# Kernel optimization log

Hardware: AMD Instinct MI355X
Metric: run time of the kernel (lower is better)

The kernel has to match this reference:

```python
import jax, jax.numpy as jnp
import numpy as np
import math

N_BREAKPOINTS = 4
V_ORDER = 2
W_ORDER = N_BREAKPOINTS - 1
B, T, C = 32, 4096, 32


def setup_inputs() -> dict:
    key = jax.random.key(0)
    k1, k2, k3 = jax.random.split(key, 3)
    x = jax.random.normal(k1, (B, T, C), dtype=jnp.float32)
    v = jax.random.normal(k2, (C, V_ORDER, T), dtype=jnp.float32)
    w = jax.random.normal(k3, (C, W_ORDER, T), dtype=jnp.float32)
    return {"x": x, "v": v, "w": w}


def reference(x, v, w):
    # x: (B, T, C); v: (C, V_ORDER, T); w: (C, W_ORDER, T)
    Bv, Tv, Cv = x.shape
    # breakpoints = T / w_order * i, i = 0..n_breakpoints-1 (as in build())
    bp = (jnp.arange(N_BREAKPOINTS, dtype=jnp.float32) * (float(Tv) / W_ORDER))
    k_lo = bp[:-1]  # (W_ORDER,) left breakpoint k_{j-1}
    k_hi = bp[1:]   # (W_ORDER,) right breakpoint k_j

    # sigma1: sum_j v[c,j,t] * x^j / j!
    powers = jnp.stack(
        [x ** j / jnp.float32(math.factorial(j)) for j in range(V_ORDER)], axis=-1
    )  # (B, T, C, V_ORDER)
    sigma1 = jnp.einsum("btcj,cjt->btc", powers, v)

    # sigma2: piecewise quadratic basis per spline segment
    xb = x[..., None]  # (B, T, C, 1)
    f1 = 0.5 * (xb - k_lo) ** 2                               # x^2/2 - k_lo*x + k_lo^2/2
    dk = k_hi - k_lo
    f2 = 0.5 * dk * dk + dk * (xb - k_hi)
    inside = (xb > k_lo) & (xb < k_hi)
    basis = jnp.where(inside, f1, f2)  # (B, T, C, W_ORDER)
    sigma2 = jnp.einsum("btck,ckt->btc", basis, w)

    return sigma1 + sigma2
```

## Files before the change

### kernel.cpp

```cpp
#include <hip/hip_runtime.h>

constexpr int B = 32, T = 4096, C = 32;
constexpr int NK = 3;
constexpr int BVEC = 4;

typedef float f32x4 __attribute__((ext_vector_type(4)));

__global__ __launch_bounds__(256) void saaf_kernel(
    const float* __restrict__ x,
    const float* __restrict__ v,
    const float* __restrict__ w,
    float* __restrict__ out)
{
    const int tid = blockIdx.x * blockDim.x + threadIdx.x;
    const int c4  = tid & 7;
    const int t   = (tid >> 3) & (T - 1);
    const int bg  = tid >> 15;
    const int c0  = c4 * 4;

    const float step = (float)(4096.0 / 3.0);
    float klo[NK], khi[NK], dk[NK], hdk2[NK];
#pragma unroll
    for (int k = 0; k < NK; ++k) {
        klo[k]  = (float)k * step;
        khi[k]  = (float)(k + 1) * step;
        dk[k]   = khi[k] - klo[k];
        hdk2[k] = (0.5f * dk[k]) * dk[k];
    }

    float v0[4], v1[4], w0[4], w1[4], w2[4];
#pragma unroll
    for (int i = 0; i < 4; ++i) {
        const int c = c0 + i;
        v0[i] = v[(c * 2 + 0) * T + t];
        v1[i] = v[(c * 2 + 1) * T + t];
        w0[i] = w[(c * 3 + 0) * T + t];
        w1[i] = w[(c * 3 + 1) * T + t];
        w2[i] = w[(c * 3 + 2) * T + t];
    }

#pragma unroll
    for (int bb = 0; bb < BVEC; ++bb) {
        const int b = bg * BVEC + bb;
        const size_t base = ((size_t)b * T + t) * C + c0;
        const f32x4 xv = __builtin_nontemporal_load((const f32x4*)&x[base]);
        float os[4];
#pragma unroll
        for (int i = 0; i < 4; ++i) {
            const float xx = xv[i];
            float acc = v0[i] + xx * v1[i];
#pragma unroll
            for (int k = 0; k < NK; ++k) {
                const float d1 = xx - klo[k];
                const float f1 = 0.5f * (d1 * d1);
                const float f2 = hdk2[k] + dk[k] * (xx - khi[k]);
                const bool inside = (xx > klo[k]) && (xx < khi[k]);
                const float basis = inside ? f1 : f2;
                const float wk = (k == 0) ? w0[i] : (k == 1) ? w1[i] : w2[i];
                acc += basis * wk;
            }
            os[i] = acc;
        }
        f32x4 ov;
        ov[0] = os[0]; ov[1] = os[1]; ov[2] = os[2]; ov[3] = os[3];
        __builtin_nontemporal_store(ov, (f32x4*)&out[base]);
    }
}

extern "C" void kernel_launch(void* const* d_in, const int* in_sizes, int n_in,
                              void* d_out, int out_size, void* d_ws, size_t ws_size,
                              hipStream_t stream) {
    const float* x = (const float*)d_in[0];
    const float* v = (const float*)d_in[1];
    const float* w = (const float*)d_in[2];
    float* out = (float*)d_out;

    const int threads = (T * (C / 4)) * (B / BVEC);
    const int block = 256;
    const int grid = threads / block;
    saaf_kernel<<<grid, block, 0, stream>>>(x, v, w, out);
}
```

Baseline: 13.34 us.

## Stage v/w coefficients through padded LDS tiles and batch x loads up front

Each block now loads a 32-timestep tile of v and w with coalesced global reads into padded shared memory, then threads read their per-channel coefficients from LDS rather than doing strided global gathers. All four x vectors are loaded before compute to expose memory-level parallelism, and the nontemporal load/store hints are replaced with plain vector accesses. This adds a __syncthreads and LDS traffic per block, and dropping the nontemporal hints may change cache behaviour.

```diff
diff --git a/kernel.cpp b/kernel.cpp
--- a/kernel.cpp
+++ b/kernel.cpp
@@ -3,6 +3,7 @@
 constexpr int B = 32, T = 4096, C = 32;
 constexpr int NK = 3;
 constexpr int BVEC = 4;
+constexpr int PAD = 33;
 
 typedef float f32x4 __attribute__((ext_vector_type(4)));
 
@@ -12,11 +13,32 @@
     const float* __restrict__ w,
     float* __restrict__ out)
 {
-    const int tid = blockIdx.x * blockDim.x + threadIdx.x;
-    const int c4  = tid & 7;
-    const int t   = (tid >> 3) & (T - 1);
-    const int bg  = tid >> 15;
-    const int c0  = c4 * 4;
+    __shared__ float lv[64 * PAD];
+    __shared__ float lw[96 * PAD];
+
+    const int tid = threadIdx.x;
+    const int bt  = blockIdx.x & 127;
+    const int bg  = blockIdx.x >> 7;
+    const int t0  = bt * 32;
+
+#pragma unroll
+    for (int i = 0; i < 8; ++i) {
+        const int idx = i * 256 + tid;
+        const int seg = idx >> 5, tl = idx & 31;
+        lv[seg * PAD + tl] = v[seg * T + t0 + tl];
+    }
+#pragma unroll
+    for (int i = 0; i < 12; ++i) {
+        const int idx = i * 256 + tid;
+        const int seg = idx >> 5, tl = idx & 31;
+        lw[seg * PAD + tl] = w[seg * T + t0 + tl];
+    }
+    __syncthreads();
+
+    const int c4 = tid & 7;
+    const int tl = tid >> 3;
+    const int c0 = c4 * 4;
+    const int t  = t0 + tl;
 
     const float step = (float)(4096.0 / 3.0);
     float klo[NK], khi[NK], dk[NK], hdk2[NK];
@@ -32,22 +54,27 @@
 #pragma unroll
     for (int i = 0; i < 4; ++i) {
         const int c = c0 + i;
-        v0[i] = v[(c * 2 + 0) * T + t];
-        v1[i] = v[(c * 2 + 1) * T + t];
-        w0[i] = w[(c * 3 + 0) * T + t];
-        w1[i] = w[(c * 3 + 1) * T + t];
-        w2[i] = w[(c * 3 + 2) * T + t];
+        v0[i] = lv[(c * 2 + 0) * PAD + tl];
+        v1[i] = lv[(c * 2 + 1) * PAD + tl];
+        w0[i] = lw[(c * 3 + 0) * PAD + tl];
+        w1[i] = lw[(c * 3 + 1) * PAD + tl];
+        w2[i] = lw[(c * 3 + 2) * PAD + tl];
+    }
+
+    f32x4 xv[BVEC];
+#pragma unroll
+    for (int bb = 0; bb < BVEC; ++bb) {
+        const int b = bg * BVEC + bb;
+        xv[bb] = *(const f32x4*)&x[((size_t)b * T + t) * C + c0];
     }
 
 #pragma unroll
     for (int bb = 0; bb < BVEC; ++bb) {
         const int b = bg * BVEC + bb;
-        const size_t base = ((size_t)b * T + t) * C + c0;
-        const f32x4 xv = __builtin_nontemporal_load((const f32x4*)&x[base]);
         float os[4];
 #pragma unroll
         for (int i = 0; i < 4; ++i) {
-            const float xx = xv[i];
+            const float xx = xv[bb][i];
             float acc = v0[i] + xx * v1[i];
 #pragma unroll
             for (int k = 0; k < NK; ++k) {
@@ -63,7 +90,7 @@
         }
         f32x4 ov;
         ov[0] = os[0]; ov[1] = os[1]; ov[2] = os[2]; ov[3] = os[3];
-        __builtin_nontemporal_store(ov, (f32x4*)&out[base]);
+        *(f32x4*)&out[((size_t)b * T + t) * C + c0] = ov;
     }
 }
 
@@ -75,8 +102,6 @@
     const float* w = (const float*)d_in[2];
     float* out = (float*)d_out;
 
-    const int threads = (T * (C / 4)) * (B / BVEC);
-    const int block = 256;
-    const int grid = threads / block;
-    saaf_kernel<<<grid, block, 0, stream>>>(x, v, w, out);
+    const int grid = (T / 32) * (B / BVEC);
+    saaf_kernel<<<grid, 256, 0, stream>>>(x, v, w, out);
 }
```

Result: faster. 11.25 us (-15.6%).
